# Kernel tuning notes

Measured on AMD Instinct MI355X. Metric: run time of the kernel, lower is better.

The kernel has to match this reference:

```python
import jax, jax.numpy as jnp
import numpy as np

H = 112; W = 112; C = 128; WS = 7; SHIFT = 3; NH = 4; B = 8
HID = 512; EPS = 1e-5
N = WS * WS
HD = C // NH
SCALE = HD ** -0.5
NW = (H // WS) * (W // WS)


def _rel_pos_index():
    coords = np.stack(np.meshgrid(np.arange(WS), np.arange(WS), indexing='ij'))  # (2,ws,ws)
    cf = coords.reshape(2, -1)
    rc = (cf[:, :, None] - cf[:, None, :]).transpose(1, 2, 0).astype(np.int64)
    rc[:, :, 0] += WS - 1
    rc[:, :, 1] += WS - 1
    rc[:, :, 0] *= 2 * WS - 1
    return jnp.asarray(rc.sum(-1))  # (N,N)


def _attn_mask():
    img = np.zeros((H, W))
    sl = (slice(0, -WS), slice(-WS, -SHIFT), slice(-SHIFT, None))
    cnt = 0
    for hs in sl:
        for ws_ in sl:
            img[hs, ws_] = cnt
            cnt += 1
    mw = img.reshape(H // WS, WS, W // WS, WS).transpose(0, 2, 1, 3).reshape(-1, N)
    am = mw[:, None, :] - mw[:, :, None]  # (nW,N,N)
    return jnp.asarray(np.where(am != 0, -100.0, 0.0), dtype=jnp.float32)


RPI = _rel_pos_index()
AMASK = _attn_mask()


def _ln(x, w, b):
    m = x.mean(-1, keepdims=True)
    v = ((x - m) ** 2).mean(-1, keepdims=True)
    return (x - m) / jnp.sqrt(v + EPS) * w + b


def _win_part(x):  # (B,H,W,C) -> (B*nW, N, C)
    b = x.shape[0]
    x = x.reshape(b, H // WS, WS, W // WS, WS, C).transpose(0, 1, 3, 2, 4, 5)
    return x.reshape(-1, N, C)


def _win_rev(wnd, b):  # (B*nW, N, C) -> (B,H,W,C)
    x = wnd.reshape(b, H // WS, W // WS, WS, WS, C).transpose(0, 1, 3, 2, 4, 5)
    return x.reshape(b, H, W, C)


def setup_inputs() -> dict:
    key = jax.random.key(0)
    ks = jax.random.split(key, 16)
    s = 0.02
    return {
        'x': jax.random.normal(ks[0], (B, H * W, C), dtype=jnp.float32),
        'saliency_gt': jnp.zeros((B, H * W, 1), dtype=jnp.float32),
        'norm1_w': jnp.ones((C,), jnp.float32),
        'norm1_b': jnp.zeros((C,), jnp.float32),
        'qkv_w': jax.random.normal(ks[1], (3 * C, C), jnp.float32) * s,
        'qkv_b': jnp.zeros((3 * C,), jnp.float32),
        'rpb_table': jax.random.normal(ks[2], ((2 * WS - 1) * (2 * WS - 1), NH), jnp.float32) * s,
        'proj_w': jax.random.normal(ks[3], (C, C), jnp.float32) * s,
        'proj_b': jnp.zeros((C,), jnp.float32),
        'norm2_w': jnp.ones((C,), jnp.float32),
        'norm2_b': jnp.zeros((C,), jnp.float32),
        'fc1_w': jax.random.normal(ks[4], (HID, C), jnp.float32) * s,
        'fc1_b': jnp.zeros((HID,), jnp.float32),
        'fc2_w': jax.random.normal(ks[5], (C, HID), jnp.float32) * s,
        'fc2_b': jnp.zeros((C,), jnp.float32),
    }


def reference(x, saliency_gt, norm1_w, norm1_b, qkv_w, qkv_b, rpb_table,
              proj_w, proj_b, norm2_w, norm2_b, fc1_w, fc1_b, fc2_w, fc2_b):
    shortcut = x  # (B, L, C)
    h = _ln(x, norm1_w, norm1_b).reshape(B, H, W, C)
    h = jnp.roll(h, (-SHIFT, -SHIFT), axis=(1, 2))  # cyclic shift
    xw = _win_part(h)  # (B*nW, N, C)
    Bn = xw.shape[0]
    qkv = (xw @ qkv_w.T + qkv_b).reshape(Bn, N, 3, NH, HD).transpose(2, 0, 3, 1, 4)
    q, k, v = qkv[0] * SCALE, qkv[1], qkv[2]  # (Bn, NH, N, HD)
    attn = jnp.einsum('bhnd,bhmd->bhnm', q, k)
    bias = rpb_table[RPI.reshape(-1)].reshape(N, N, NH).transpose(2, 0, 1)  # (NH,N,N)
    attn = attn + bias[None]
    attn = attn.reshape(B, NW, NH, N, N) + AMASK[None, :, None]
    attn = jax.nn.softmax(attn.reshape(Bn, NH, N, N), axis=-1)
    out = jnp.einsum('bhnm,bhmd->bhnd', attn, v).transpose(0, 2, 1, 3).reshape(Bn, N, C)
    out = out @ proj_w.T + proj_b
    h = _win_rev(out, B)
    h = jnp.roll(h, (SHIFT, SHIFT), axis=(1, 2)).reshape(B, H * W, C)
    x = shortcut + h
    y = _ln(x, norm2_w, norm2_b)
    y = jax.nn.gelu(y @ fc1_w.T + fc1_b, approximate=False)
    y = y @ fc2_w.T + fc2_b
    return x + y
```

## Files before the change

kernel.cpp:

```cpp
#include <hip/hip_runtime.h>


using ubf    = unsigned short;
using short8 = __attribute__((ext_vector_type(8))) short;
using bf16x8 = __attribute__((ext_vector_type(8))) __bf16;
using f32x4  = __attribute__((ext_vector_type(4))) float;

#define LL 12544
#define CC 128
#define SCALE_Q 0.17677669529663687f
#define F32PAT 0x3F800000u
#define XST 136
#define QKST 40
#define PST 72
#define VST 72

__device__ __forceinline__ float b2f(ubf u) { return __uint_as_float(((unsigned)u) << 16); }
__device__ __forceinline__ ubf   f2b(float f) {
  unsigned u = __float_as_uint(f);
  return (ubf)((u + 0x7fffu + ((u >> 16) & 1u)) >> 16);
}
__device__ __forceinline__ f32x4 zero4() { f32x4 z = {0.f, 0.f, 0.f, 0.f}; return z; }
__device__ __forceinline__ f32x4 mfma_b(short8 a, short8 b, f32x4 c) {
  return __builtin_amdgcn_mfma_f32_16x16x32_bf16(
      __builtin_bit_cast(bf16x8, a), __builtin_bit_cast(bf16x8, b), c, 0, 0, 0);
}
__device__ __forceinline__ float gelu_f(float v) {
  float t = v * (1.5957691216057308f + 0.0713548162726f * v * v);
  t = fminf(t, 80.f);
  float e = __expf(t);
  return v * __fdividef(e, 1.f + e);
}

struct CvtT { const void* src; int dst; int cnt; };
struct CvtArgs { CvtT t[8]; };
struct SwzT { const void* src; int dst; int cnt; int kw; int kkb; };
struct SwzArgs { SwzT t[4]; };

__global__ __launch_bounds__(256) void k_prep(CvtArgs a, SwzArgs sj,
                                              const unsigned* __restrict__ probe,
                                              ubf* __restrict__ cw,
                                              ubf* __restrict__ swz,
                                              const void* __restrict__ rpb,
                                              float* __restrict__ bias) {
  bool f32 = (probe[0] == F32PAT);
  int blk = blockIdx.x, tid = threadIdx.x;
  if (blk < 8) {
    const CvtT& t = a.t[blk];
#pragma unroll
    for (int it = 0; it < 2; ++it) {
      int o = tid + it * 256;
      if (o < t.cnt) {
        float v = f32 ? ((const float*)t.src)[o] : b2f(((const ubf*)t.src)[o]);
        cw[t.dst + o] = f2b(v);
      }
    }
  } else if (blk < 46) {
    int idx = (blk - 8) * 256 + tid;
    if (idx >= 4 * 49 * 49) return;
    int h = idx / 2401;
    int rem = idx - h * 2401;
    int n = rem / 49, m = rem - n * 49;
    int iq = n / 7, jq = n - iq * 7, ik = m / 7, jk = m - ik * 7;
    int rpi = (iq - ik + 6) * 13 + (jq - jk + 6);
    bias[idx] = f32 ? ((const float*)rpb)[rpi * 4 + h] : b2f(((const ubf*)rpb)[rpi * 4 + h]);
  } else {
    int idx = (blk - 46) * 256 + tid;
#pragma unroll
    for (int t = 0; t < 4; ++t) {
      int o = idx - sj.t[t].dst;
      if (o >= 0 && o < sj.t[t].cnt) {
        int e = o & 7, lane = (o >> 3) & 63;
        int kk = (o >> 9) & ((1 << sj.t[t].kkb) - 1);
        int tn = o >> (9 + sj.t[t].kkb);
        int row = lane & 15, quad = lane >> 4;
        int si = (tn * 16 + row) * sj.t[t].kw + kk * 32 + quad * 8 + e;
        float v = f32 ? ((const float*)sj.t[t].src)[si] : b2f(((const ubf*)sj.t[t].src)[si]);
        swz[idx] = f2b(v);
      }
    }
  }
}

__global__ __launch_bounds__(256, 2) void k_fused(const void* __restrict__ x,
                                                  const unsigned* __restrict__ probe,
                                                  const ubf* __restrict__ n1w,
                                                  const ubf* __restrict__ n1b,
                                                  const ubf* __restrict__ qkvw,
                                                  const ubf* __restrict__ qkvb,
                                                  const float* __restrict__ bias,
                                                  const ubf* __restrict__ pw,
                                                  const ubf* __restrict__ pb,
                                                  ubf* __restrict__ x2) {
  __shared__ __align__(16) ubf sm[38400];
  __shared__ int cls[49];
  int tid = threadIdx.x, win = blockIdx.x;
  int bb = win >> 8, w2 = win & 255, wr = w2 >> 4, wc = w2 & 15;
  bool f32 = (probe[0] == F32PAT);

  if (tid < 49) {
    int i = tid / 7, j = tid - i * 7;
    int rr = wr * 7 + i, cc = wc * 7 + j;
    int ra = (rr < 105) ? 0 : (rr < 109 ? 1 : 2);
    int ca = (cc < 105) ? 0 : (cc < 109 ? 1 : 2);
    cls[tid] = ra * 3 + ca;
  }

  {
    int rowt = tid >> 2, sub = tid & 3;
    ubf* xd = sm + rowt * XST + sub * 32;
    if (rowt < 49) {
      int i = rowt / 7, j = rowt - i * 7;
      int rr = wr * 7 + i + 3; if (rr >= 112) rr -= 112;
      int cc = wc * 7 + j + 3; if (cc >= 112) cc -= 112;
      size_t src = ((size_t)bb * LL + rr * 112 + cc) * CC + sub * 32;
      float v[32];
      if (f32) {
        const float* xp = (const float*)x + src;
#pragma unroll
        for (int q = 0; q < 8; ++q) {
          float4 p = *(const float4*)(xp + q * 4);
          v[q * 4] = p.x; v[q * 4 + 1] = p.y; v[q * 4 + 2] = p.z; v[q * 4 + 3] = p.w;
        }
      } else {
        const ubf* xp = (const ubf*)x + src;
#pragma unroll
        for (int q = 0; q < 4; ++q) {
          short8 p = *(const short8*)(xp + q * 8);
#pragma unroll
          for (int e = 0; e < 8; ++e) v[q * 8 + e] = b2f((ubf)p[e]);
        }
      }
      float s = 0.f, sq = 0.f;
#pragma unroll
      for (int e = 0; e < 32; ++e) { s += v[e]; sq += v[e] * v[e]; }
      s += __shfl_xor(s, 1, 64);  sq += __shfl_xor(sq, 1, 64);
      s += __shfl_xor(s, 2, 64);  sq += __shfl_xor(sq, 2, 64);
      float mean = s * (1.f / 128.f);
      float var  = sq * (1.f / 128.f) - mean * mean;
      float rstd = rsqrtf(var + 1e-5f);
#pragma unroll
      for (int q = 0; q < 4; ++q) {
        short8 wv = *(const short8*)(n1w + sub * 32 + q * 8);
        short8 bv = *(const short8*)(n1b + sub * 32 + q * 8);
        short8 o;
#pragma unroll
        for (int e = 0; e < 8; ++e)
          o[e] = (short)f2b((v[q * 8 + e] - mean) * rstd * b2f((ubf)wv[e]) + b2f((ubf)bv[e]));
        *(short8*)(xd + q * 8) = o;
      }
    } else {
      short8 z = {0, 0, 0, 0, 0, 0, 0, 0};
#pragma unroll
      for (int q = 0; q < 4; ++q) *(short8*)(xd + q * 8) = z;
    }
  }
  __syncthreads();

  int wid = tid >> 6, lane = tid & 63;
  int row = lane & 15, quad = lane >> 4;
  int head = wid;
  ubf* qI = sm + 8704 + wid * 5120;
  ubf* kI = qI + 2560;
  ubf* Pt = qI;
  ubf* vT = sm + 29184 + wid * 2304;

  int nb[6] = {32 * wid, 32 * wid + 16, 128 + 32 * wid, 128 + 32 * wid + 16,
               256 + 32 * wid, 256 + 32 * wid + 16};
  f32x4 acc[4][6];
#pragma unroll
  for (int tm = 0; tm < 4; ++tm)
#pragma unroll
    for (int tn = 0; tn < 6; ++tn) acc[tm][tn] = zero4();
#pragma unroll
  for (int k0 = 0; k0 < 128; k0 += 32) {
    int kk = k0 >> 5;
    short8 a[4], bw[6];
#pragma unroll
    for (int tm = 0; tm < 4; ++tm)
      a[tm] = *(const short8*)&sm[(tm * 16 + row) * XST + k0 + quad * 8];
#pragma unroll
    for (int tn = 0; tn < 6; ++tn)
      bw[tn] = *(const short8*)(qkvw + (((nb[tn] >> 4) * 4 + kk) << 9) + (lane << 3));
#pragma unroll
    for (int tm = 0; tm < 4; ++tm)
#pragma unroll
      for (int tn = 0; tn < 6; ++tn) acc[tm][tn] = mfma_b(a[tm], bw[tn], acc[tm][tn]);
  }

  float qkb[6];
#pragma unroll
  for (int tn = 0; tn < 6; ++tn) qkb[tn] = b2f(qkvb[nb[tn] + row]);
#pragma unroll
  for (int tm = 0; tm < 4; ++tm)
#pragma unroll
    for (int r = 0; r < 4; ++r) {
      int tok = tm * 16 + quad * 4 + r;
#pragma unroll
      for (int tn = 0; tn < 2; ++tn)
        qI[tok * QKST + tn * 16 + row] = f2b((acc[tm][tn][r] + qkb[tn]) * SCALE_Q);
#pragma unroll
      for (int tn = 2; tn < 4; ++tn)
        kI[tok * QKST + (tn - 2) * 16 + row] = f2b(acc[tm][tn][r] + qkb[tn]);
    }
#pragma unroll
  for (int tm = 0; tm < 4; ++tm)
#pragma unroll
    for (int tn = 4; tn < 6; ++tn) {
      unsigned lo = (unsigned)f2b(acc[tm][tn][0] + qkb[tn]) |
                    ((unsigned)f2b(acc[tm][tn][1] + qkb[tn]) << 16);
      unsigned hi = (unsigned)f2b(acc[tm][tn][2] + qkb[tn]) |
                    ((unsigned)f2b(acc[tm][tn][3] + qkb[tn]) << 16);
      uint2 pk; pk.x = lo; pk.y = hi;
      *(uint2*)&vT[((tn - 4) * 16 + row) * VST + tm * 16 + quad * 4] = pk;
    }

  short8 aq[4], bk[4];
#pragma unroll
  for (int tm = 0; tm < 4; ++tm)
    aq[tm] = *(const short8*)&qI[(tm * 16 + row) * QKST + quad * 8];
#pragma unroll
  for (int tn = 0; tn < 4; ++tn)
    bk[tn] = *(const short8*)&kI[(tn * 16 + row) * QKST + quad * 8];

  f32x4 S[4][4];
#pragma unroll
  for (int tm = 0; tm < 4; ++tm)
#pragma unroll
    for (int tn = 0; tn < 4; ++tn) S[tm][tn] = zero4();
#pragma unroll
  for (int tm = 0; tm < 4; ++tm)
#pragma unroll
    for (int tn = 0; tn < 4; ++tn) S[tm][tn] = mfma_b(aq[tm], bk[tn], S[tm][tn]);

  int kcls[4];
  bool kval[4];
#pragma unroll
  for (int tn = 0; tn < 4; ++tn) {
    int key = tn * 16 + row;
    kval[tn] = key < 49;
    kcls[tn] = kval[tn] ? cls[key] : 0;
  }
  float inv[4][4];
#pragma unroll
  for (int tm = 0; tm < 4; ++tm)
#pragma unroll
    for (int r = 0; r < 4; ++r) {
      int qy = tm * 16 + quad * 4 + r;
      bool qv = qy < 49;
      int qc = qv ? cls[qy] : 0;
      const float* brow = bias + ((size_t)(head * 49 + (qv ? qy : 0))) * 49;
      float sum = 0.f;
#pragma unroll
      for (int tn = 0; tn < 4; ++tn) {
        int key = tn * 16 + row;
        float p;
        if (qv && kval[tn]) {
          float s = S[tm][tn][r] + brow[key];
          if (kcls[tn] != qc) s -= 100.0f;
          p = __expf(fminf(s, 60.f));
        } else {
          p = 0.f;
        }
        Pt[qy * PST + key] = f2b(p);
        sum += p;
      }
      sum += __shfl_xor(sum, 1, 64);
      sum += __shfl_xor(sum, 2, 64);
      sum += __shfl_xor(sum, 4, 64);
      sum += __shfl_xor(sum, 8, 64);
      inv[tm][r] = qv ? __fdividef(1.f, sum) : 0.f;
    }

  f32x4 O[4][2];
#pragma unroll
  for (int tm = 0; tm < 4; ++tm)
#pragma unroll
    for (int tn = 0; tn < 2; ++tn) O[tm][tn] = zero4();
#pragma unroll
  for (int ks = 0; ks < 2; ++ks) {
    short8 av[4], bv[2];
#pragma unroll
    for (int tm = 0; tm < 4; ++tm)
      av[tm] = *(const short8*)&Pt[(tm * 16 + row) * PST + ks * 32 + quad * 8];
#pragma unroll
    for (int tn = 0; tn < 2; ++tn)
      bv[tn] = *(const short8*)&vT[(tn * 16 + row) * VST + ks * 32 + quad * 8];
#pragma unroll
    for (int tm = 0; tm < 4; ++tm)
#pragma unroll
      for (int tn = 0; tn < 2; ++tn) O[tm][tn] = mfma_b(av[tm], bv[tn], O[tm][tn]);
  }
#pragma unroll
  for (int tm = 0; tm < 4; ++tm)
#pragma unroll
    for (int tn = 0; tn < 2; ++tn)
#pragma unroll
      for (int r = 0; r < 4; ++r) O[tm][tn][r] *= inv[tm][r];

  __syncthreads();

#pragma unroll
  for (int tm = 0; tm < 4; ++tm)
#pragma unroll
    for (int r = 0; r < 4; ++r) {
      int qy = tm * 16 + quad * 4 + r;
#pragma unroll
      for (int tn = 0; tn < 2; ++tn)
        sm[qy * XST + head * 32 + tn * 16 + row] = f2b(O[tm][tn][r]);
    }
  __syncthreads();

  {
    f32x4 pacc[4][2];
#pragma unroll
    for (int tm = 0; tm < 4; ++tm)
#pragma unroll
      for (int tn = 0; tn < 2; ++tn) pacc[tm][tn] = zero4();
#pragma unroll
    for (int k0 = 0; k0 < 128; k0 += 32) {
      int kk = k0 >> 5;
      short8 a[4], bw[2];
#pragma unroll
      for (int tm = 0; tm < 4; ++tm)
        a[tm] = *(const short8*)&sm[(tm * 16 + row) * XST + k0 + quad * 8];
#pragma unroll
      for (int tn = 0; tn < 2; ++tn)
        bw[tn] = *(const short8*)(pw + (((wid * 2 + tn) * 4 + kk) << 9) + (lane << 3));
#pragma unroll
      for (int tm = 0; tm < 4; ++tm)
#pragma unroll
        for (int tn = 0; tn < 2; ++tn) pacc[tm][tn] = mfma_b(a[tm], bw[tn], pacc[tm][tn]);
    }
    int n0p = wid * 32;
#pragma unroll
    for (int tm = 0; tm < 4; ++tm)
#pragma unroll
      for (int r = 0; r < 4; ++r) {
        int m = tm * 16 + quad * 4 + r;
        if (m < 49) {
          int i = m / 7, j = m - i * 7;
          int rr = wr * 7 + i + 3; if (rr >= 112) rr -= 112;
          int cc = wc * 7 + j + 3; if (cc >= 112) cc -= 112;
          size_t l = (size_t)bb * LL + rr * 112 + cc;
#pragma unroll
          for (int tn = 0; tn < 2; ++tn) {
            int n = n0p + tn * 16 + row;
            float xv = f32 ? ((const float*)x)[l * 128 + n] : b2f(((const ubf*)x)[l * 128 + n]);
            x2[l * 128 + n] = f2b(pacc[tm][tn][r] + b2f(pb[n]) + xv);
          }
        }
      }
  }
}

__global__ __launch_bounds__(256, 4) void k_mlp(const ubf* __restrict__ x2,
                                                const ubf* __restrict__ n2w,
                                                const ubf* __restrict__ n2b,
                                                const ubf* __restrict__ f1w,
                                                const ubf* __restrict__ f1b,
                                                const ubf* __restrict__ f2w,
                                                const ubf* __restrict__ f2b_,
                                                float* __restrict__ out) {
  __shared__ __align__(16) ubf xln[4096];
  __shared__ __align__(16) ubf h1s[16384];
  int m0 = blockIdx.x * 32;
  int tid = threadIdx.x;

  {
    int row = tid >> 3, sub = tid & 7;
    const ubf* xr = x2 + (size_t)(m0 + row) * 128 + sub * 16;
    short8 p0 = *(const short8*)(xr);
    short8 p1 = *(const short8*)(xr + 8);
    float v[16];
#pragma unroll
    for (int i = 0; i < 8; ++i) { v[i] = b2f((ubf)p0[i]); v[8 + i] = b2f((ubf)p1[i]); }
    float s = 0.f, sq = 0.f;
#pragma unroll
    for (int i = 0; i < 16; ++i) { s += v[i]; sq += v[i] * v[i]; }
#pragma unroll
    for (int m = 1; m < 8; m <<= 1) {
      s += __shfl_xor(s, m, 64);
      sq += __shfl_xor(sq, m, 64);
    }
    float mean = s * (1.f / 128.f);
    float var  = sq * (1.f / 128.f) - mean * mean;
    float rstd = rsqrtf(var + 1e-5f);
    short8 w0 = *(const short8*)(n2w + sub * 16);
    short8 w1 = *(const short8*)(n2w + sub * 16 + 8);
    short8 b0 = *(const short8*)(n2b + sub * 16);
    short8 b1 = *(const short8*)(n2b + sub * 16 + 8);
    short8 o0, o1;
#pragma unroll
    for (int i = 0; i < 8; ++i) {
      o0[i] = (short)f2b((v[i] - mean) * rstd * b2f((ubf)w0[i]) + b2f((ubf)b0[i]));
      o1[i] = (short)f2b((v[8 + i] - mean) * rstd * b2f((ubf)w1[i]) + b2f((ubf)b1[i]));
    }
    int b0i = row * 128 + sub * 16;
    int swx = (row & 7) << 3;
    *(short8*)(xln + (b0i ^ swx)) = o0;
    *(short8*)(xln + ((b0i + 8) ^ swx)) = o1;
  }
  __syncthreads();

  int wid = tid >> 6, lane = tid & 63;
  int row = lane & 15, quad = lane >> 4;
  int swr = (row & 7) << 3;

#pragma unroll
  for (int nt = 0; nt < 2; ++nt) {
    short8 bwAll[4][4];
#pragma unroll
    for (int kk = 0; kk < 4; ++kk)
#pragma unroll
      for (int tn = 0; tn < 4; ++tn)
        bwAll[kk][tn] = *(const short8*)(f1w +
            (((wid * 8 + nt * 4 + tn) * 4 + kk) << 9) + (lane << 3));
    f32x4 acc[2][4];
#pragma unroll
    for (int tm = 0; tm < 2; ++tm)
#pragma unroll
      for (int tn = 0; tn < 4; ++tn) acc[tm][tn] = zero4();
#pragma unroll
    for (int kk = 0; kk < 4; ++kk) {
      short8 a[2];
#pragma unroll
      for (int tm = 0; tm < 2; ++tm)
        a[tm] = *(const short8*)&xln[((tm * 16 + row) * 128 + kk * 32 + quad * 8) ^ swr];
#pragma unroll
      for (int tm = 0; tm < 2; ++tm)
#pragma unroll
        for (int tn = 0; tn < 4; ++tn) acc[tm][tn] = mfma_b(a[tm], bwAll[kk][tn], acc[tm][tn]);
    }
    int n0 = wid * 128 + nt * 64;
#pragma unroll
    for (int tm = 0; tm < 2; ++tm)
#pragma unroll
      for (int r = 0; r < 4; ++r) {
        int m = tm * 16 + quad * 4 + r;
#pragma unroll
        for (int tn = 0; tn < 4; ++tn) {
          int n = n0 + tn * 16 + row;
          h1s[(m * 512 + n) ^ ((m & 7) << 3)] = f2b(gelu_f(acc[tm][tn][r] + b2f(f1b[n])));
        }
      }
  }
  __syncthreads();

  {
    int n0 = wid * 32;
    f32x4 acc[2][2];
#pragma unroll
    for (int tm = 0; tm < 2; ++tm)
#pragma unroll
      for (int tn = 0; tn < 2; ++tn) acc[tm][tn] = zero4();
#pragma unroll
    for (int kg = 0; kg < 4; ++kg) {
      short8 bw2[4][2], a2[4][2];
#pragma unroll
      for (int kk = 0; kk < 4; ++kk)
#pragma unroll
        for (int tn = 0; tn < 2; ++tn)
          bw2[kk][tn] = *(const short8*)(f2w +
              (((wid * 2 + tn) * 16 + kg * 4 + kk) << 9) + (lane << 3));
#pragma unroll
      for (int kk = 0; kk < 4; ++kk)
#pragma unroll
        for (int tm = 0; tm < 2; ++tm)
          a2[kk][tm] = *(const short8*)&h1s[
              (((tm * 16 + row) * 512 + (kg * 4 + kk) * 32 + quad * 8)) ^ swr];
#pragma unroll
      for (int kk = 0; kk < 4; ++kk)
#pragma unroll
        for (int tm = 0; tm < 2; ++tm)
#pragma unroll
          for (int tn = 0; tn < 2; ++tn)
            acc[tm][tn] = mfma_b(a2[kk][tm], bw2[kk][tn], acc[tm][tn]);
    }
#pragma unroll
    for (int tm = 0; tm < 2; ++tm)
#pragma unroll
      for (int r = 0; r < 4; ++r) {
        int m = tm * 16 + quad * 4 + r;
#pragma unroll
        for (int tn = 0; tn < 2; ++tn) {
          int n = n0 + tn * 16 + row;
          float vv = acc[tm][tn][r] + b2f(f2b_[n]) + b2f(x2[(size_t)(m0 + m) * 128 + n]);
          out[(size_t)(m0 + m) * 128 + n] = vv;
        }
      }
  }
}

extern "C" void kernel_launch(void* const* d_in, const int* in_sizes, int n_in,
                              void* d_out, int out_size, void* d_ws, size_t ws_size,
                              hipStream_t stream) {
  const unsigned* probe = (const unsigned*)d_in[2];

  char* ws = (char*)d_ws;
  ubf*   swz  = (ubf*)(ws + 0);
  ubf*   x2   = (ubf*)(ws + 136314880);
  ubf*   cw   = (ubf*)(ws + 162004992);
  float* bias = (float*)(ws + 162404992);

  ubf *n1w = cw + 0,     *n1b = cw + 128,   *qkvb = cw + 49408;
  ubf *pb = cw + 66856;
  ubf *n2w = cw + 66984, *n2b = cw + 67112, *f1b = cw + 132776, *f2b_ = cw + 198824;

  ubf *qkvw_s = swz + 0;
  ubf *pw_s   = swz + 49152;
  ubf *f1w_s  = swz + 65536;
  ubf *f2w_s  = swz + 131072;

  CvtArgs ca;
  const int sidx[8] = {2, 3, 5, 8, 9, 10, 12, 14};
  const int sdst[8] = {0, 128, 49408, 66856, 66984, 67112, 132776, 198824};
  const int scnt[8] = {128, 128, 384, 128, 128, 128, 512, 128};
  for (int t = 0; t < 8; ++t) {
    ca.t[t].src = d_in[sidx[t]];
    ca.t[t].dst = sdst[t];
    ca.t[t].cnt = scnt[t];
  }

  SwzArgs sa;
  const int widx[4] = {4, 7, 11, 13};
  const int wdst[4] = {0, 49152, 65536, 131072};
  const int wcnt[4] = {49152, 16384, 65536, 65536};
  const int wkw[4]  = {128, 128, 128, 512};
  const int wkb[4]  = {2, 2, 2, 4};
  for (int t = 0; t < 4; ++t) {
    sa.t[t].src = d_in[widx[t]];
    sa.t[t].dst = wdst[t];
    sa.t[t].cnt = wcnt[t];
    sa.t[t].kw  = wkw[t];
    sa.t[t].kkb = wkb[t];
  }

  k_prep<<<dim3(814), dim3(256), 0, stream>>>(ca, sa, probe, cw, swz, d_in[6], bias);
  k_fused<<<dim3(2048), dim3(256), 0, stream>>>(d_in[0], probe, n1w, n1b, qkvw_s, qkvb,
                                                bias, pw_s, pb, x2);
  k_mlp<<<dim3(3136), dim3(256), 0, stream>>>(x2, n2w, n2b, f1w_s, f1b, f2w_s, f2b_,
                                              (float*)d_out);
}
```

Before: 247.7 us.

## Keep V in registers via shuffles, shrink LDS, raise occupancy to 4 blocks

The V^T staging buffer and the mask-class array are removed from LDS. V is packed into bf16 registers with v_cvt_pk_bf16_f32 and redistributed into the MFMA B-operand layout with cross-lane shuffles, and mask classes are fetched by shuffle from a per-lane register. Q/K scratch now reuses the input tile region after an added barrier, which cuts shared memory from about 77KB to 40KB, and launch bounds go to 4 blocks per CU. The score tiles are computed one row-tile at a time to lower register pressure. In exchange it adds many shuffles and an extra barrier, and the tighter register budget may cause spills.

```diff
diff --git a/kernel.cpp b/kernel.cpp
--- a/kernel.cpp
+++ b/kernel.cpp
@@ -13,12 +13,16 @@
 #define XST 136
 #define QKST 40
 #define PST 72
-#define VST 72
 
 __device__ __forceinline__ float b2f(ubf u) { return __uint_as_float(((unsigned)u) << 16); }
 __device__ __forceinline__ ubf   f2b(float f) {
   unsigned u = __float_as_uint(f);
   return (ubf)((u + 0x7fffu + ((u >> 16) & 1u)) >> 16);
+}
+__device__ __forceinline__ unsigned cvtpk(float lo, float hi) {
+  unsigned r;
+  asm volatile("v_cvt_pk_bf16_f32 %0, %1, %2" : "=v"(r) : "v"(lo), "v"(hi));
+  return r;
 }
 __device__ __forceinline__ f32x4 zero4() { f32x4 z = {0.f, 0.f, 0.f, 0.f}; return z; }
 __device__ __forceinline__ f32x4 mfma_b(short8 a, short8 b, f32x4 c) {
@@ -82,7 +86,7 @@
   }
 }
 
-__global__ __launch_bounds__(256, 2) void k_fused(const void* __restrict__ x,
+__global__ __launch_bounds__(256, 4) void k_fused(const void* __restrict__ x,
                                                   const unsigned* __restrict__ probe,
                                                   const ubf* __restrict__ n1w,
                                                   const ubf* __restrict__ n1b,
@@ -92,18 +96,23 @@
                                                   const ubf* __restrict__ pw,
                                                   const ubf* __restrict__ pb,
                                                   ubf* __restrict__ x2) {
-  __shared__ __align__(16) ubf sm[38400];
-  __shared__ int cls[49];
+  __shared__ __align__(16) ubf sm[20480];
   int tid = threadIdx.x, win = blockIdx.x;
   int bb = win >> 8, w2 = win & 255, wr = w2 >> 4, wc = w2 & 15;
   bool f32 = (probe[0] == F32PAT);
 
-  if (tid < 49) {
-    int i = tid / 7, j = tid - i * 7;
+  int wid = tid >> 6, lane = tid & 63;
+  int row = lane & 15, quad = lane >> 4;
+
+  int clsReg;
+  {
+    int t = lane;
+    int i = (t * 9363) >> 16;
+    int j = t - i * 7;
     int rr = wr * 7 + i, cc = wc * 7 + j;
     int ra = (rr < 105) ? 0 : (rr < 109 ? 1 : 2);
     int ca = (cc < 105) ? 0 : (cc < 109 ? 1 : 2);
-    cls[tid] = ra * 3 + ca;
+    clsReg = ra * 3 + ca;
   }
 
   {
@@ -157,13 +166,10 @@
   }
   __syncthreads();
 
-  int wid = tid >> 6, lane = tid & 63;
-  int row = lane & 15, quad = lane >> 4;
   int head = wid;
-  ubf* qI = sm + 8704 + wid * 5120;
+  ubf* qI = sm + wid * 5120;
   ubf* kI = qI + 2560;
   ubf* Pt = qI;
-  ubf* vT = sm + 29184 + wid * 2304;
 
   int nb[6] = {32 * wid, 32 * wid + 16, 128 + 32 * wid, 128 + 32 * wid + 16,
                256 + 32 * wid, 256 + 32 * wid + 16};
@@ -191,6 +197,19 @@
   float qkb[6];
 #pragma unroll
   for (int tn = 0; tn < 6; ++tn) qkb[tn] = b2f(qkvb[nb[tn] + row]);
+
+  unsigned pkV[4][2][2];
+#pragma unroll
+  for (int tm = 0; tm < 4; ++tm)
+#pragma unroll
+    for (int tv = 0; tv < 2; ++tv) {
+      float b = qkb[4 + tv];
+      pkV[tm][tv][0] = cvtpk(acc[tm][4 + tv][0] + b, acc[tm][4 + tv][1] + b);
+      pkV[tm][tv][1] = cvtpk(acc[tm][4 + tv][2] + b, acc[tm][4 + tv][3] + b);
+    }
+
+  __syncthreads();
+
 #pragma unroll
   for (int tm = 0; tm < 4; ++tm)
 #pragma unroll
@@ -203,17 +222,6 @@
       for (int tn = 2; tn < 4; ++tn)
         kI[tok * QKST + (tn - 2) * 16 + row] = f2b(acc[tm][tn][r] + qkb[tn]);
     }
-#pragma unroll
-  for (int tm = 0; tm < 4; ++tm)
-#pragma unroll
-    for (int tn = 4; tn < 6; ++tn) {
-      unsigned lo = (unsigned)f2b(acc[tm][tn][0] + qkb[tn]) |
-                    ((unsigned)f2b(acc[tm][tn][1] + qkb[tn]) << 16);
-      unsigned hi = (unsigned)f2b(acc[tm][tn][2] + qkb[tn]) |
-                    ((unsigned)f2b(acc[tm][tn][3] + qkb[tn]) << 16);
-      uint2 pk; pk.x = lo; pk.y = hi;
-      *(uint2*)&vT[((tn - 4) * 16 + row) * VST + tm * 16 + quad * 4] = pk;
-    }
 
   short8 aq[4], bk[4];
 #pragma unroll
@@ -222,16 +230,6 @@
 #pragma unroll
   for (int tn = 0; tn < 4; ++tn)
     bk[tn] = *(const short8*)&kI[(tn * 16 + row) * QKST + quad * 8];
-
-  f32x4 S[4][4];
-#pragma unroll
-  for (int tm = 0; tm < 4; ++tm)
-#pragma unroll
-    for (int tn = 0; tn < 4; ++tn) S[tm][tn] = zero4();
-#pragma unroll
-  for (int tm = 0; tm < 4; ++tm)
-#pragma unroll
-    for (int tn = 0; tn < 4; ++tn) S[tm][tn] = mfma_b(aq[tm], bk[tn], S[tm][tn]);
 
   int kcls[4];
   bool kval[4];
@@ -239,16 +237,20 @@
   for (int tn = 0; tn < 4; ++tn) {
     int key = tn * 16 + row;
     kval[tn] = key < 49;
-    kcls[tn] = kval[tn] ? cls[key] : 0;
-  }
+    kcls[tn] = __shfl(clsReg, key);
+  }
+
   float inv[4][4];
 #pragma unroll
-  for (int tm = 0; tm < 4; ++tm)
+  for (int tm = 0; tm < 4; ++tm) {
+    f32x4 S[4];
+#pragma unroll
+    for (int tn = 0; tn < 4; ++tn) S[tn] = mfma_b(aq[tm], bk[tn], zero4());
 #pragma unroll
     for (int r = 0; r < 4; ++r) {
       int qy = tm * 16 + quad * 4 + r;
       bool qv = qy < 49;
-      int qc = qv ? cls[qy] : 0;
+      int qc = __shfl(clsReg, qy);
       const float* brow = bias + ((size_t)(head * 49 + (qv ? qy : 0))) * 49;
       float sum = 0.f;
 #pragma unroll
@@ -256,7 +258,7 @@
         int key = tn * 16 + row;
         float p;
         if (qv && kval[tn]) {
-          float s = S[tm][tn][r] + brow[key];
+          float s = S[tn][r] + brow[key];
           if (kcls[tn] != qc) s -= 100.0f;
           p = __expf(fminf(s, 60.f));
         } else {
@@ -271,6 +273,7 @@
       sum += __shfl_xor(sum, 8, 64);
       inv[tm][r] = qv ? __fdividef(1.f, sum) : 0.f;
     }
+  }
 
   f32x4 O[4][2];
 #pragma unroll
@@ -284,8 +287,18 @@
     for (int tm = 0; tm < 4; ++tm)
       av[tm] = *(const short8*)&Pt[(tm * 16 + row) * PST + ks * 32 + quad * 8];
 #pragma unroll
-    for (int tn = 0; tn < 2; ++tn)
-      bv[tn] = *(const short8*)&vT[(tn * 16 + row) * VST + ks * 32 + quad * 8];
+    for (int tn = 0; tn < 2; ++tn) {
+      unsigned w[4];
+#pragma unroll
+      for (int p = 0; p < 4; ++p) {
+        int sl = row + 16 * (((quad & 1) << 1) + (p >> 1));
+        int lo = __shfl((int)pkV[2 * ks][tn][p & 1], sl);
+        int hi = __shfl((int)pkV[2 * ks + 1][tn][p & 1], sl);
+        w[p] = (unsigned)((quad & 2) ? hi : lo);
+      }
+      uint4 uw; uw.x = w[0]; uw.y = w[1]; uw.z = w[2]; uw.w = w[3];
+      bv[tn] = __builtin_bit_cast(short8, uw);
+    }
 #pragma unroll
     for (int tm = 0; tm < 4; ++tm)
 #pragma unroll
```

New measurement: 296.7 us. +19.8%, slower.
